# Kernel tuning notes

Measured on AMD Instinct MI355X. Metric: run time of the kernel, lower is better.

## Reference

```python
import jax, jax.numpy as jnp
import numpy as np

N_NODES = 50000
N_EDGES = 800000
HIDDEN = 128
N_LAYERS = 3
EPS = 1e-5


def setup_inputs() -> dict:
    key = jax.random.key(0)
    ks = jax.random.split(key, 6)
    x = jax.random.normal(ks[0], (N_NODES, HIDDEN), dtype=jnp.float32)
    edge_index = jax.random.randint(ks[1], (2, N_EDGES), 0, N_NODES, dtype=jnp.int64)
    scale = 1.0 / np.sqrt(HIDDEN)
    Wl = jax.random.normal(ks[2], (N_LAYERS, HIDDEN, HIDDEN), dtype=jnp.float32) * scale
    bl = jnp.zeros((N_LAYERS, HIDDEN), dtype=jnp.float32)
    Wr = jax.random.normal(ks[3], (N_LAYERS, HIDDEN, HIDDEN), dtype=jnp.float32) * scale
    gamma = jnp.ones((N_LAYERS, HIDDEN), dtype=jnp.float32)
    beta = jnp.zeros((N_LAYERS, HIDDEN), dtype=jnp.float32)
    return {"x": x, "edge_index": edge_index, "Wl": Wl, "bl": bl,
            "Wr": Wr, "gamma": gamma, "beta": beta}


def reference(x, edge_index, Wl, bl, Wr, gamma, beta):
    # SAGEConv (mean aggr): out_i = Wl @ mean_{j in N(i)} x_j + bl + Wr @ x_i
    # followed by BatchNorm (batch stats), ReLU, residual (layers > 0).
    src, dst = edge_index[0], edge_index[1]
    N = x.shape[0]
    deg = jax.ops.segment_sum(jnp.ones((src.shape[0],), dtype=x.dtype), dst,
                              num_segments=N)
    inv_deg = (1.0 / jnp.maximum(deg, 1.0))[:, None]  # [N,1]; empty nbhd -> 0 agg
    for i in range(N_LAYERS):
        msg = x[src]                                            # [E,H] gather
        agg = jax.ops.segment_sum(msg, dst, num_segments=N) * inv_deg  # [N,H]
        h = agg @ Wl[i].T + bl[i] + x @ Wr[i].T                 # [N,H]
        mean = jnp.mean(h, axis=0)
        var = jnp.var(h, axis=0)                                # biased, as torch BN
        h = gamma[i] * (h - mean) * jax.lax.rsqrt(var + EPS) + beta[i]
        h = jax.nn.relu(h)
        x = h + x if i > 0 else h
    return x
```

## Files before the change

kernel.cpp:

```cpp
#include <hip/hip_runtime.h>

#define HH 128
#define EPS 1e-5f
#define NBMAX 256
#define SCAP 40
#define FCAP 12288

typedef __bf16 bf16x8 __attribute__((ext_vector_type(8)));
typedef float f32x4 __attribute__((ext_vector_type(4)));
typedef float f32x2 __attribute__((ext_vector_type(2)));

__device__ __forceinline__ unsigned f2bf(float f) {
    unsigned u = __builtin_bit_cast(unsigned, f);
    return (u + 0x7FFFu + ((u >> 16) & 1u)) >> 16;
}
__device__ __forceinline__ float bflo(unsigned w) { return __builtin_bit_cast(float, w << 16); }
__device__ __forceinline__ float bfhi(unsigned w) { return __builtin_bit_cast(float, w & 0xFFFF0000u); }

__device__ __forceinline__ unsigned pack_fp8x4(float f0, float f1, float f2, float f3) {
    unsigned r = 0;
    r = __builtin_amdgcn_cvt_pk_fp8_f32(f0, f1, r, false);
    r = __builtin_amdgcn_cvt_pk_fp8_f32(f2, f3, r, true);
    return r;
}

__device__ __forceinline__ void gload_lds16(const void* g, void* l) {
    __builtin_amdgcn_global_load_lds(
        (const __attribute__((address_space(1))) unsigned int*)g,
        (__attribute__((address_space(3))) unsigned int*)l,
        16, 0, 0);
}

__global__ void zero_small_kernel(int* __restrict__ bcnt, float* __restrict__ stats3,
                                  unsigned* __restrict__ bar3) {
    const int t = threadIdx.x;
    bcnt[t] = 0;
    stats3[t] = 0.f; stats3[256 + t] = 0.f; stats3[512 + t] = 0.f;
    if (t < 3) bar3[t] = 0u;
}

__global__ __launch_bounds__(256) void bucket_hist_kernel(const int* __restrict__ dst,
                                                          int* __restrict__ bcnt, int E) {
    __shared__ int h[NBMAX];
    const int t = threadIdx.x;
    h[t] = 0;
    __syncthreads();
    for (int e = blockIdx.x * 256 + t; e < E; e += gridDim.x * 256)
        atomicAdd(&h[dst[e] >> 8], 1);
    __syncthreads();
    if (h[t]) atomicAdd(&bcnt[t], h[t]);
}

__global__ __launch_bounds__(256) void bucket_scan_kernel(const int* __restrict__ bcnt,
                                                          int* __restrict__ boff,
                                                          int* __restrict__ gpos, int NB, int E) {
    __shared__ int s[NBMAX];
    const int t = threadIdx.x;
    s[t] = (t < NB) ? bcnt[t] : 0;
    __syncthreads();
    for (int off = 1; off < 256; off <<= 1) {
        int u = (t >= off) ? s[t - off] : 0;
        __syncthreads();
        s[t] += u;
        __syncthreads();
    }
    int excl = (t == 0) ? 0 : s[t - 1];
    if (t < NB) { boff[t] = excl; gpos[t] = excl; }
    if (t == 0) boff[NB] = E;
}

__global__ __launch_bounds__(256) void bucket_scatter_kernel(
    const int* __restrict__ src, const int* __restrict__ dst,
    int* __restrict__ gpos, unsigned* __restrict__ packed, int E, int GRID)
{
    __shared__ unsigned q[NBMAX][SCAP];
    __shared__ int qc[NBMAX];
    const int t = threadIdx.x;
    const int b = blockIdx.x;
    qc[t] = 0;
    __syncthreads();
    const int ebeg = (int)((long)b * E / GRID);
    const int eend = (int)((long)(b + 1) * E / GRID);
    for (int base = ebeg; base < eend; base += 256) {
        int e = base + t;
        if (e < eend) {
            int d = dst[e];
            unsigned pk = ((unsigned)d << 16) | (unsigned)src[e];
            int bk = d >> 8;
            int slot = atomicAdd(&qc[bk], 1);
            if (slot < SCAP) q[bk][slot] = pk;
            else { int p = atomicAdd(&gpos[bk], 1); packed[p] = pk; }
        }
        __syncthreads();
        int c = qc[t]; if (c > SCAP) c = SCAP;
        if (c >= 32) {
            int p = atomicAdd(&gpos[t], 32);
            for (int i = 0; i < 32; ++i) packed[p + i] = q[t][i];
            for (int i = 32; i < c; ++i) q[t][i - 32] = q[t][i];
            qc[t] = c - 32;
        } else {
            qc[t] = c;
        }
        __syncthreads();
    }
    int c = qc[t]; if (c > SCAP) c = SCAP;
    if (c > 0) {
        int p = atomicAdd(&gpos[t], c);
        for (int i = 0; i < c; ++i) packed[p + i] = q[t][i];
    }
}

__global__ __launch_bounds__(256) void bucket_finalize_kernel(
    const unsigned* __restrict__ packed, const int* __restrict__ boff,
    int* __restrict__ row_ptr, float* __restrict__ invdeg,
    ushort* __restrict__ edge_csr, int N, int E)
{
    __shared__ int hist[256];
    __shared__ int posq[256];
    __shared__ ushort outq[FCAP];
    const int b = blockIdx.x, t = threadIdx.x;
    const int beg = boff[b], end = boff[b + 1], n = end - beg;
    hist[t] = 0;
    __syncthreads();
    for (int i = beg + t; i < end; i += 256)
        atomicAdd(&hist[(packed[i] >> 16) & 255], 1);
    __syncthreads();
    const int c = hist[t];
    for (int off = 1; off < 256; off <<= 1) {
        int u = (t >= off) ? hist[t - off] : 0;
        __syncthreads();
        hist[t] += u;
        __syncthreads();
    }
    const int excl = hist[t] - c;
    const int node = (b << 8) + t;
    if (node < N) {
        row_ptr[node] = beg + excl;
        invdeg[node] = 1.0f / fmaxf((float)c, 1.0f);
    }
    if (b == 0 && t == 0) row_ptr[N] = E;
    posq[t] = excl;
    __syncthreads();
    if (n <= FCAP) {
        for (int i = beg + t; i < end; i += 256) {
            unsigned pk = packed[i];
            int p = atomicAdd(&posq[(pk >> 16) & 255], 1);
            outq[p] = (ushort)(pk & 0xFFFFu);
        }
        __syncthreads();
        for (int i = t; i < n; i += 256) edge_csr[beg + i] = outq[i];
    } else {
        for (int i = beg + t; i < end; i += 256) {
            unsigned pk = packed[i];
            int p = atomicAdd(&posq[(pk >> 16) & 255], 1);
            edge_csr[beg + p] = (ushort)(pk & 0xFFFFu);
        }
    }
}

__global__ void convert_all_kernel(const float* __restrict__ x,
                                   const float* __restrict__ Wl, const float* __restrict__ Wr,
                                   ushort* __restrict__ xb, unsigned* __restrict__ xq,
                                   ushort* __restrict__ Wb,
                                   int n4, int m4, int wtotal) {
    int gid = blockIdx.x * 256 + threadIdx.x;
    if (gid < wtotal) {
        int l = gid / (HH * 256);
        int rem = gid - l * (HH * 256);
        int col = rem >> 8;
        int k = rem & 255;
        float v = (k < HH) ? Wl[(size_t)l * HH * HH + col * HH + k]
                           : Wr[(size_t)l * HH * HH + col * HH + (k - HH)];
        Wb[gid] = (ushort)f2bf(v);
        return;
    }
    int idx = gid - wtotal;
    if (idx >= m4) return;
    uint2 o = make_uint2(0u, 0u);
    unsigned q = 0u;
    if (idx < n4) {
        float4 v = ((const float4*)x)[idx];
        o.x = f2bf(v.x) | (f2bf(v.y) << 16);
        o.y = f2bf(v.z) | (f2bf(v.w) << 16);
        q = pack_fp8x4(v.x, v.y, v.z, v.w);
    }
    ((uint2*)xb)[idx] = o;
    xq[idx] = q;
}

__global__ __launch_bounds__(256) void gather_kernel(
    const unsigned* __restrict__ xq, const int* __restrict__ row_ptr,
    const ushort* __restrict__ edge_csr, const float* __restrict__ invdeg,
    ushort* __restrict__ aggb, int N)
{
    const int node = blockIdx.x * 16 + (threadIdx.x >> 4);
    const int l16 = threadIdx.x & 15;
    float a0=0,a1=0,a2=0,a3=0,a4=0,a5=0,a6=0,a7=0;
    float id = 0.f;
    if (node < N) {
        const int beg = row_ptr[node], end = row_ptr[node + 1];
        id = invdeg[node];
        int e = beg;
        for (; e + 3 < end; e += 4) {
            int s0 = edge_csr[e], s1 = edge_csr[e + 1];
            int s2 = edge_csr[e + 2], s3 = edge_csr[e + 3];
            uint2 v0 = *(const uint2*)(xq + (size_t)s0 * 32 + l16 * 2);
            uint2 v1 = *(const uint2*)(xq + (size_t)s1 * 32 + l16 * 2);
            uint2 v2 = *(const uint2*)(xq + (size_t)s2 * 32 + l16 * 2);
            uint2 v3 = *(const uint2*)(xq + (size_t)s3 * 32 + l16 * 2);
            f32x2 p;
            p = __builtin_amdgcn_cvt_pk_f32_fp8(v0.x, false); a0 += p.x; a1 += p.y;
            p = __builtin_amdgcn_cvt_pk_f32_fp8(v0.x, true);  a2 += p.x; a3 += p.y;
            p = __builtin_amdgcn_cvt_pk_f32_fp8(v0.y, false); a4 += p.x; a5 += p.y;
            p = __builtin_amdgcn_cvt_pk_f32_fp8(v0.y, true);  a6 += p.x; a7 += p.y;
            p = __builtin_amdgcn_cvt_pk_f32_fp8(v1.x, false); a0 += p.x; a1 += p.y;
            p = __builtin_amdgcn_cvt_pk_f32_fp8(v1.x, true);  a2 += p.x; a3 += p.y;
            p = __builtin_amdgcn_cvt_pk_f32_fp8(v1.y, false); a4 += p.x; a5 += p.y;
            p = __builtin_amdgcn_cvt_pk_f32_fp8(v1.y, true);  a6 += p.x; a7 += p.y;
            p = __builtin_amdgcn_cvt_pk_f32_fp8(v2.x, false); a0 += p.x; a1 += p.y;
            p = __builtin_amdgcn_cvt_pk_f32_fp8(v2.x, true);  a2 += p.x; a3 += p.y;
            p = __builtin_amdgcn_cvt_pk_f32_fp8(v2.y, false); a4 += p.x; a5 += p.y;
            p = __builtin_amdgcn_cvt_pk_f32_fp8(v2.y, true);  a6 += p.x; a7 += p.y;
            p = __builtin_amdgcn_cvt_pk_f32_fp8(v3.x, false); a0 += p.x; a1 += p.y;
            p = __builtin_amdgcn_cvt_pk_f32_fp8(v3.x, true);  a2 += p.x; a3 += p.y;
            p = __builtin_amdgcn_cvt_pk_f32_fp8(v3.y, false); a4 += p.x; a5 += p.y;
            p = __builtin_amdgcn_cvt_pk_f32_fp8(v3.y, true);  a6 += p.x; a7 += p.y;
        }
        for (; e < end; ++e) {
            int s0 = edge_csr[e];
            uint2 v0 = *(const uint2*)(xq + (size_t)s0 * 32 + l16 * 2);
            f32x2 p;
            p = __builtin_amdgcn_cvt_pk_f32_fp8(v0.x, false); a0 += p.x; a1 += p.y;
            p = __builtin_amdgcn_cvt_pk_f32_fp8(v0.x, true);  a2 += p.x; a3 += p.y;
            p = __builtin_amdgcn_cvt_pk_f32_fp8(v0.y, false); a4 += p.x; a5 += p.y;
            p = __builtin_amdgcn_cvt_pk_f32_fp8(v0.y, true);  a6 += p.x; a7 += p.y;
        }
    }
    uint4 o;
    o.x = f2bf(a0 * id) | (f2bf(a1 * id) << 16);
    o.y = f2bf(a2 * id) | (f2bf(a3 * id) << 16);
    o.z = f2bf(a4 * id) | (f2bf(a5 * id) << 16);
    o.w = f2bf(a6 * id) | (f2bf(a7 * id) << 16);
    *(uint4*)(aggb + (size_t)node * HH + l16 * 8) = o;
}

__global__ __launch_bounds__(512) void fused_layer_kernel(
    const ushort* __restrict__ aggb, ushort* __restrict__ xb,
    const ushort* __restrict__ Wb, const float* __restrict__ bl,
    const float* __restrict__ gamma, const float* __restrict__ beta,
    float* __restrict__ stats, unsigned* __restrict__ bar,
    unsigned* __restrict__ xq, float* __restrict__ outf,
    float invN, int nblocks, int N, int residual, int final_layer)
{
    extern __shared__ ushort As[];
    __shared__ float s_sum[128];
    __shared__ float s_sum2[128];

    const int tid = threadIdx.x;
    const int lane = tid & 63;
    const int wave = tid >> 6;
    const int m0 = blockIdx.x * 256;
    const int l15 = lane & 15;
    const int lg = lane >> 4;
    const int col = wave * 16 + l15;

#pragma unroll
    for (int i = 0; i < 16; ++i) {
        const int cb = (i * 8 + wave) * 64;
        const int L = cb + lane;
        const int r = L >> 5;
        const int c = L & 31;
        const int cs = (c & 0x18) | ((c & 7) ^ (r & 7));
        const ushort* gsrc = (cs < 16)
            ? (aggb + (size_t)(m0 + r) * HH + cs * 8)
            : (xb   + (size_t)(m0 + r) * HH + (cs - 16) * 8);
        gload_lds16(gsrc, &As[(size_t)cb * 8]);
    }

    bf16x8 bfr[8];
#pragma unroll
    for (int s = 0; s < 8; ++s)
        bfr[s] = *(const bf16x8*)(Wb + (size_t)col * 256 + s * 32 + lg * 8);

    if (tid < 128) { s_sum[tid] = 0.f; s_sum2[tid] = 0.f; }

    f32x4 acc[16];
#pragma unroll
    for (int rt = 0; rt < 16; ++rt) acc[rt] = (f32x4){0.f, 0.f, 0.f, 0.f};

    __syncthreads();

#pragma unroll
    for (int s = 0; s < 8; ++s) {
#pragma unroll
        for (int rt = 0; rt < 16; ++rt) {
            const int r = rt * 16 + l15;
            const int g = s * 4 + lg;
            const int c = (g & 0x18) | ((g & 7) ^ (r & 7));
            bf16x8 a = *(const bf16x8*)&As[r * 256 + c * 8];
            acc[rt] = __builtin_amdgcn_mfma_f32_16x16x32_bf16(a, bfr[s], acc[rt], 0, 0, 0);
        }
    }

    const float bias = bl[col];
    float s1 = 0.f, s2 = 0.f;
#pragma unroll
    for (int rt = 0; rt < 16; ++rt) {
#pragma unroll
        for (int r = 0; r < 4; ++r) {
            const int row = rt * 16 + lg * 4 + r;
            if (m0 + row < N) {
                float v = acc[rt][r] + bias;
                s1 += v; s2 += v * v;
            }
        }
    }
    atomicAdd(&s_sum[col], s1);
    atomicAdd(&s_sum2[col], s2);
    __syncthreads();
    if (tid < 128) {
        atomicAdd(&stats[tid], s_sum[tid]);
        atomicAdd(&stats[128 + tid], s_sum2[tid]);
    }
    if (tid == 0) {
        __threadfence();
        __hip_atomic_fetch_add(bar, 1u, __ATOMIC_ACQ_REL, __HIP_MEMORY_SCOPE_AGENT);
        while (__hip_atomic_load(bar, __ATOMIC_ACQUIRE, __HIP_MEMORY_SCOPE_AGENT) < (unsigned)nblocks)
            __builtin_amdgcn_s_sleep(8);
    }
    __syncthreads();

    const float sA = __hip_atomic_load(&stats[col], __ATOMIC_RELAXED, __HIP_MEMORY_SCOPE_AGENT);
    const float sB = __hip_atomic_load(&stats[128 + col], __ATOMIC_RELAXED, __HIP_MEMORY_SCOPE_AGENT);
    const float mean = sA * invN;
    const float var = sB * invN - mean * mean;
    const float aa = gamma[col] * rsqrtf(var + EPS);
    const float bb = beta[col] - mean * aa;

    ushort* Cs = As;
#pragma unroll
    for (int rt = 0; rt < 16; ++rt) {
#pragma unroll
        for (int r = 0; r < 4; ++r) {
            const int row = rt * 16 + lg * 4 + r;
            float v = acc[rt][r] + bias;
            float o = fmaxf(fmaf(v, aa, bb), 0.f);
            Cs[row * 136 + col] = (ushort)f2bf(o);
        }
    }
    __syncthreads();

#pragma unroll
    for (int i = 0; i < 8; ++i) {
        const int ch = tid + i * 512;
        const int row = ch >> 4;
        const int q = ch & 15;
        const int grow = m0 + row;
        if (grow < N) {
            uint4 v = *(const uint4*)&Cs[row * 136 + q * 8];
            float o0 = bflo(v.x), o1 = bfhi(v.x);
            float o2 = bflo(v.y), o3 = bfhi(v.y);
            float o4 = bflo(v.z), o5 = bfhi(v.z);
            float o6 = bflo(v.w), o7 = bfhi(v.w);
            if (residual) {
                uint4 xw = *(const uint4*)(xb + (size_t)grow * HH + q * 8);
                o0 += bflo(xw.x); o1 += bfhi(xw.x);
                o2 += bflo(xw.y); o3 += bfhi(xw.y);
                o4 += bflo(xw.z); o5 += bfhi(xw.z);
                o6 += bflo(xw.w); o7 += bfhi(xw.w);
            }
            if (final_layer) {
                float* op = outf + (size_t)grow * HH + q * 8;
                *(float4*)op = make_float4(o0, o1, o2, o3);
                *(float4*)(op + 4) = make_float4(o4, o5, o6, o7);
            } else {
                uint4 ob;
                ob.x = f2bf(o0) | (f2bf(o1) << 16);
                ob.y = f2bf(o2) | (f2bf(o3) << 16);
                ob.z = f2bf(o4) | (f2bf(o5) << 16);
                ob.w = f2bf(o6) | (f2bf(o7) << 16);
                *(uint4*)(xb + (size_t)grow * HH + q * 8) = ob;
                uint2 qb;
                qb.x = pack_fp8x4(o0, o1, o2, o3);
                qb.y = pack_fp8x4(o4, o5, o6, o7);
                *(uint2*)(xq + (size_t)grow * 32 + q * 2) = qb;
            }
        }
    }
}

extern "C" void kernel_launch(void* const* d_in, const int* in_sizes, int n_in,
                              void* d_out, int out_size, void* d_ws, size_t ws_size,
                              hipStream_t stream) {
    const float* x     = (const float*)d_in[0];
    const int*   ei    = (const int*)d_in[1];
    const float* Wl    = (const float*)d_in[2];
    const float* bl    = (const float*)d_in[3];
    const float* Wr    = (const float*)d_in[4];
    const float* gamma = (const float*)d_in[5];
    const float* beta  = (const float*)d_in[6];
    float* out = (float*)d_out;

    const int N = in_sizes[0] / HH;
    const int E = in_sizes[1] / 2;
    const int MP = ((N + 255) / 256) * 256;
    const int NB = (N + 255) >> 8;
    const int* src = ei;
    const int* dst = ei + E;

    char* p = (char*)d_ws;
    ushort* aggb    = (ushort*)p; p += (size_t)MP * HH * 2;
    ushort* xb      = (ushort*)p; p += (size_t)MP * HH * 2;
    unsigned* xq    = (unsigned*)p; p += (size_t)MP * 32 * 4;
    ushort* Wb      = (ushort*)p; p += (size_t)3 * HH * 256 * 2;
    float* invdeg   = (float*)p;  p += (size_t)N * 4;
    float* stats3   = (float*)p;  p += 768 * 4;
    unsigned* bar3  = (unsigned*)p; p += 16 * 4;
    int* row_ptr    = (int*)p;    p += (size_t)(N + 4) * 4;
    int* bcnt       = (int*)p;    p += NBMAX * 4;
    int* boff       = (int*)p;    p += (NBMAX + 1) * 4;
    int* gpos       = (int*)p;    p += NBMAX * 4;
    unsigned* packed = (unsigned*)p; p += (size_t)E * 4;
    ushort* edge_csr = (ushort*)p;  p += (size_t)((E + 7) & ~7) * 2;

    hipFuncSetAttribute((const void*)fused_layer_kernel,
                        hipFuncAttributeMaxDynamicSharedMemorySize, 131072);

    zero_small_kernel<<<1, 256, 0, stream>>>(bcnt, stats3, bar3);
    bucket_hist_kernel<<<512, 256, 0, stream>>>(dst, bcnt, E);
    bucket_scan_kernel<<<1, 256, 0, stream>>>(bcnt, boff, gpos, NB, E);
    bucket_scatter_kernel<<<256, 256, 0, stream>>>(src, dst, gpos, packed, E, 256);
    bucket_finalize_kernel<<<NB, 256, 0, stream>>>(packed, boff, row_ptr, invdeg, edge_csr, N, E);

    const int wtotal = 3 * HH * 256;
    const int n4 = N * (HH / 4);
    const int m4 = MP * (HH / 4);
    convert_all_kernel<<<(wtotal + m4 + 255) / 256, 256, 0, stream>>>(
        x, Wl, Wr, xb, xq, Wb, n4, m4, wtotal);

    const int gather_blocks = MP / 16;
    const int fused_blocks = MP / 256;

    for (int layer = 0; layer < 3; ++layer) {
        gather_kernel<<<gather_blocks, 256, 0, stream>>>(
            xq, row_ptr, edge_csr, invdeg, aggb, N);

        fused_layer_kernel<<<fused_blocks, 512, 131072, stream>>>(
            aggb, xb, Wb + (size_t)layer * HH * 256, bl + (size_t)layer * HH,
            gamma + (size_t)layer * HH, beta + (size_t)layer * HH,
            stats3 + layer * 256, bar3 + layer,
            xq, out, 1.0f / (float)N, fused_blocks, N,
            layer > 0 ? 1 : 0, layer == 2 ? 1 : 0);
    }
}
```

Before: 223.3 us.

## Merge CSR build and conversion prologue into one persistent kernel with grid barriers

```diff
diff --git a/kernel.cpp b/kernel.cpp
--- a/kernel.cpp
+++ b/kernel.cpp
@@ -5,6 +5,7 @@
 #define NBMAX 256
 #define SCAP 40
 #define FCAP 12288
+#define MGRID 256
 
 typedef __bf16 bf16x8 __attribute__((ext_vector_type(8)));
 typedef float f32x4 __attribute__((ext_vector_type(4)));
@@ -31,161 +32,176 @@
         16, 0, 0);
 }
 
+__device__ __forceinline__ void grid_barrier(unsigned* ctr, unsigned nb) {
+    __syncthreads();
+    if (threadIdx.x == 0) {
+        __threadfence();
+        __hip_atomic_fetch_add(ctr, 1u, __ATOMIC_ACQ_REL, __HIP_MEMORY_SCOPE_AGENT);
+        while (__hip_atomic_load(ctr, __ATOMIC_ACQUIRE, __HIP_MEMORY_SCOPE_AGENT) < nb)
+            __builtin_amdgcn_s_sleep(8);
+    }
+    __syncthreads();
+}
+
+__device__ __forceinline__ int aload(const int* p) {
+    return __hip_atomic_load((int*)p, __ATOMIC_RELAXED, __HIP_MEMORY_SCOPE_AGENT);
+}
+
 __global__ void zero_small_kernel(int* __restrict__ bcnt, float* __restrict__ stats3,
-                                  unsigned* __restrict__ bar3) {
+                                  unsigned* __restrict__ bar) {
     const int t = threadIdx.x;
     bcnt[t] = 0;
     stats3[t] = 0.f; stats3[256 + t] = 0.f; stats3[512 + t] = 0.f;
-    if (t < 3) bar3[t] = 0u;
-}
-
-__global__ __launch_bounds__(256) void bucket_hist_kernel(const int* __restrict__ dst,
-                                                          int* __restrict__ bcnt, int E) {
-    __shared__ int h[NBMAX];
-    const int t = threadIdx.x;
-    h[t] = 0;
-    __syncthreads();
-    for (int e = blockIdx.x * 256 + t; e < E; e += gridDim.x * 256)
-        atomicAdd(&h[dst[e] >> 8], 1);
-    __syncthreads();
-    if (h[t]) atomicAdd(&bcnt[t], h[t]);
-}
-
-__global__ __launch_bounds__(256) void bucket_scan_kernel(const int* __restrict__ bcnt,
-                                                          int* __restrict__ boff,
-                                                          int* __restrict__ gpos, int NB, int E) {
-    __shared__ int s[NBMAX];
-    const int t = threadIdx.x;
-    s[t] = (t < NB) ? bcnt[t] : 0;
-    __syncthreads();
-    for (int off = 1; off < 256; off <<= 1) {
-        int u = (t >= off) ? s[t - off] : 0;
-        __syncthreads();
-        s[t] += u;
-        __syncthreads();
-    }
-    int excl = (t == 0) ? 0 : s[t - 1];
-    if (t < NB) { boff[t] = excl; gpos[t] = excl; }
-    if (t == 0) boff[NB] = E;
-}
-
-__global__ __launch_bounds__(256) void bucket_scatter_kernel(
+    if (t < 8) bar[t] = 0u;
+}
+
+__global__ __launch_bounds__(256) void mega_prologue_kernel(
+    const float* __restrict__ x, const float* __restrict__ Wl, const float* __restrict__ Wr,
     const int* __restrict__ src, const int* __restrict__ dst,
-    int* __restrict__ gpos, unsigned* __restrict__ packed, int E, int GRID)
+    ushort* __restrict__ xb, unsigned* __restrict__ xq, ushort* __restrict__ Wb,
+    int* __restrict__ bcnt, int* __restrict__ boff, int* __restrict__ gpos,
+    unsigned* __restrict__ packed, int* __restrict__ row_ptr,
+    float* __restrict__ invdeg, ushort* __restrict__ edge_csr,
+    unsigned* __restrict__ bar,
+    int n4, int m4, int wtotal, int N, int E, int NB)
 {
-    __shared__ unsigned q[NBMAX][SCAP];
-    __shared__ int qc[NBMAX];
+    __shared__ char smraw[NBMAX * SCAP * 4 + NBMAX * 4];
     const int t = threadIdx.x;
     const int b = blockIdx.x;
-    qc[t] = 0;
-    __syncthreads();
-    const int ebeg = (int)((long)b * E / GRID);
-    const int eend = (int)((long)(b + 1) * E / GRID);
-    for (int base = ebeg; base < eend; base += 256) {
-        int e = base + t;
-        if (e < eend) {
-            int d = dst[e];
-            unsigned pk = ((unsigned)d << 16) | (unsigned)src[e];
-            int bk = d >> 8;
-            int slot = atomicAdd(&qc[bk], 1);
-            if (slot < SCAP) q[bk][slot] = pk;
-            else { int p = atomicAdd(&gpos[bk], 1); packed[p] = pk; }
-        }
-        __syncthreads();
-        int c = qc[t]; if (c > SCAP) c = SCAP;
-        if (c >= 32) {
-            int p = atomicAdd(&gpos[t], 32);
-            for (int i = 0; i < 32; ++i) packed[p + i] = q[t][i];
-            for (int i = 32; i < c; ++i) q[t][i - 32] = q[t][i];
-            qc[t] = c - 32;
-        } else {
-            qc[t] = c;
-        }
-        __syncthreads();
-    }
-    int c = qc[t]; if (c > SCAP) c = SCAP;
-    if (c > 0) {
-        int p = atomicAdd(&gpos[t], c);
-        for (int i = 0; i < c; ++i) packed[p + i] = q[t][i];
-    }
-}
-
-__global__ __launch_bounds__(256) void bucket_finalize_kernel(
-    const unsigned* __restrict__ packed, const int* __restrict__ boff,
-    int* __restrict__ row_ptr, float* __restrict__ invdeg,
-    ushort* __restrict__ edge_csr, int N, int E)
-{
-    __shared__ int hist[256];
-    __shared__ int posq[256];
-    __shared__ ushort outq[FCAP];
-    const int b = blockIdx.x, t = threadIdx.x;
-    const int beg = boff[b], end = boff[b + 1], n = end - beg;
-    hist[t] = 0;
-    __syncthreads();
-    for (int i = beg + t; i < end; i += 256)
-        atomicAdd(&hist[(packed[i] >> 16) & 255], 1);
-    __syncthreads();
-    const int c = hist[t];
-    for (int off = 1; off < 256; off <<= 1) {
-        int u = (t >= off) ? hist[t - off] : 0;
-        __syncthreads();
-        hist[t] += u;
-        __syncthreads();
-    }
-    const int excl = hist[t] - c;
-    const int node = (b << 8) + t;
-    if (node < N) {
-        row_ptr[node] = beg + excl;
-        invdeg[node] = 1.0f / fmaxf((float)c, 1.0f);
-    }
-    if (b == 0 && t == 0) row_ptr[N] = E;
-    posq[t] = excl;
-    __syncthreads();
-    if (n <= FCAP) {
-        for (int i = beg + t; i < end; i += 256) {
-            unsigned pk = packed[i];
-            int p = atomicAdd(&posq[(pk >> 16) & 255], 1);
-            outq[p] = (ushort)(pk & 0xFFFFu);
-        }
-        __syncthreads();
-        for (int i = t; i < n; i += 256) edge_csr[beg + i] = outq[i];
-    } else {
-        for (int i = beg + t; i < end; i += 256) {
-            unsigned pk = packed[i];
-            int p = atomicAdd(&posq[(pk >> 16) & 255], 1);
-            edge_csr[beg + p] = (ushort)(pk & 0xFFFFu);
-        }
-    }
-}
-
-__global__ void convert_all_kernel(const float* __restrict__ x,
-                                   const float* __restrict__ Wl, const float* __restrict__ Wr,
-                                   ushort* __restrict__ xb, unsigned* __restrict__ xq,
-                                   ushort* __restrict__ Wb,
-                                   int n4, int m4, int wtotal) {
-    int gid = blockIdx.x * 256 + threadIdx.x;
-    if (gid < wtotal) {
-        int l = gid / (HH * 256);
-        int rem = gid - l * (HH * 256);
+    const int gt = b * 256 + t;
+    const int gstride = MGRID * 256;
+
+    {
+        int* h0 = (int*)smraw;
+        h0[t] = 0;
+        __syncthreads();
+        for (int e = gt; e < E; e += gstride) atomicAdd(&h0[dst[e] >> 8], 1);
+        __syncthreads();
+        if (h0[t]) atomicAdd(&bcnt[t], h0[t]);
+    }
+    for (int i = gt; i < wtotal; i += gstride) {
+        int l = i / (HH * 256);
+        int rem = i - l * (HH * 256);
         int col = rem >> 8;
         int k = rem & 255;
         float v = (k < HH) ? Wl[(size_t)l * HH * HH + col * HH + k]
                            : Wr[(size_t)l * HH * HH + col * HH + (k - HH)];
-        Wb[gid] = (ushort)f2bf(v);
-        return;
-    }
-    int idx = gid - wtotal;
-    if (idx >= m4) return;
-    uint2 o = make_uint2(0u, 0u);
-    unsigned q = 0u;
-    if (idx < n4) {
-        float4 v = ((const float4*)x)[idx];
-        o.x = f2bf(v.x) | (f2bf(v.y) << 16);
-        o.y = f2bf(v.z) | (f2bf(v.w) << 16);
-        q = pack_fp8x4(v.x, v.y, v.z, v.w);
-    }
-    ((uint2*)xb)[idx] = o;
-    xq[idx] = q;
+        Wb[i] = (ushort)f2bf(v);
+    }
+    for (int i = gt; i < m4; i += gstride) {
+        uint2 o = make_uint2(0u, 0u);
+        unsigned qv = 0u;
+        if (i < n4) {
+            float4 v = ((const float4*)x)[i];
+            o.x = f2bf(v.x) | (f2bf(v.y) << 16);
+            o.y = f2bf(v.z) | (f2bf(v.w) << 16);
+            qv = pack_fp8x4(v.x, v.y, v.z, v.w);
+        }
+        ((uint2*)xb)[i] = o;
+        xq[i] = qv;
+    }
+
+    grid_barrier(bar + 0, MGRID);
+
+    if (b == 0) {
+        int* s = (int*)smraw;
+        s[t] = (t < NB) ? aload(&bcnt[t]) : 0;
+        __syncthreads();
+        for (int off = 1; off < 256; off <<= 1) {
+            int u = (t >= off) ? s[t - off] : 0;
+            __syncthreads();
+            s[t] += u;
+            __syncthreads();
+        }
+        int excl = (t == 0) ? 0 : s[t - 1];
+        if (t < NB) { boff[t] = excl; gpos[t] = excl; }
+        if (t == 0) boff[NB] = E;
+    }
+
+    grid_barrier(bar + 1, MGRID);
+
+    {
+        unsigned (*q)[SCAP] = (unsigned (*)[SCAP])smraw;
+        int* qc = (int*)(smraw + NBMAX * SCAP * 4);
+        qc[t] = 0;
+        __syncthreads();
+        const int ebeg = (int)((long)b * E / MGRID);
+        const int eend = (int)((long)(b + 1) * E / MGRID);
+        for (int base = ebeg; base < eend; base += 256) {
+            int e = base + t;
+            if (e < eend) {
+                int d = dst[e];
+                unsigned pk = ((unsigned)d << 16) | (unsigned)src[e];
+                int bk = d >> 8;
+                int slot = atomicAdd(&qc[bk], 1);
+                if (slot < SCAP) q[bk][slot] = pk;
+                else { int p = atomicAdd(&gpos[bk], 1); packed[p] = pk; }
+            }
+            __syncthreads();
+            int c = qc[t]; if (c > SCAP) c = SCAP;
+            if (c >= 32) {
+                int p = atomicAdd(&gpos[t], 32);
+                for (int i = 0; i < 32; ++i) packed[p + i] = q[t][i];
+                for (int i = 32; i < c; ++i) q[t][i - 32] = q[t][i];
+                qc[t] = c - 32;
+            } else {
+                qc[t] = c;
+            }
+            __syncthreads();
+        }
+        int c = qc[t]; if (c > SCAP) c = SCAP;
+        if (c > 0) {
+            int p = atomicAdd(&gpos[t], c);
+            for (int i = 0; i < c; ++i) packed[p + i] = q[t][i];
+        }
+    }
+
+    grid_barrier(bar + 2, MGRID);
+
+    if (b < NB) {
+        int* hist = (int*)smraw;
+        int* posq = hist + 256;
+        ushort* outq = (ushort*)(posq + 256);
+        const int beg = aload(&boff[b]);
+        const int end = aload(&boff[b + 1]);
+        const int n = end - beg;
+        hist[t] = 0;
+        __syncthreads();
+        for (int i = beg + t; i < end; i += 256)
+            atomicAdd(&hist[(packed[i] >> 16) & 255], 1);
+        __syncthreads();
+        const int c = hist[t];
+        for (int off = 1; off < 256; off <<= 1) {
+            int u = (t >= off) ? hist[t - off] : 0;
+            __syncthreads();
+            hist[t] += u;
+            __syncthreads();
+        }
+        const int excl = hist[t] - c;
+        const int node = (b << 8) + t;
+        if (node < N) {
+            row_ptr[node] = beg + excl;
+            invdeg[node] = 1.0f / fmaxf((float)c, 1.0f);
+        }
+        if (b == 0 && t == 0) row_ptr[N] = E;
+        posq[t] = excl;
+        __syncthreads();
+        if (n <= FCAP) {
+            for (int i = beg + t; i < end; i += 256) {
+                unsigned pk = packed[i];
+                int p = atomicAdd(&posq[(pk >> 16) & 255], 1);
+                outq[p] = (ushort)(pk & 0xFFFFu);
+            }
+            __syncthreads();
+            for (int i = t; i < n; i += 256) edge_csr[beg + i] = outq[i];
+        } else {
+            for (int i = beg + t; i < end; i += 256) {
+                unsigned pk = packed[i];
+                int p = atomicAdd(&posq[(pk >> 16) & 255], 1);
+                edge_csr[beg + p] = (ushort)(pk & 0xFFFFu);
+            }
+        }
+    }
 }
 
 __global__ __launch_bounds__(256) void gather_kernel(
@@ -415,7 +431,7 @@
     ushort* Wb      = (ushort*)p; p += (size_t)3 * HH * 256 * 2;
     float* invdeg   = (float*)p;  p += (size_t)N * 4;
     float* stats3   = (float*)p;  p += 768 * 4;
-    unsigned* bar3  = (unsigned*)p; p += 16 * 4;
+    unsigned* bar   = (unsigned*)p; p += 16 * 4;
     int* row_ptr    = (int*)p;    p += (size_t)(N + 4) * 4;
     int* bcnt       = (int*)p;    p += NBMAX * 4;
     int* boff       = (int*)p;    p += (NBMAX + 1) * 4;
@@ -426,17 +442,15 @@
     hipFuncSetAttribute((const void*)fused_layer_kernel,
                         hipFuncAttributeMaxDynamicSharedMemorySize, 131072);
 
-    zero_small_kernel<<<1, 256, 0, stream>>>(bcnt, stats3, bar3);
-    bucket_hist_kernel<<<512, 256, 0, stream>>>(dst, bcnt, E);
-    bucket_scan_kernel<<<1, 256, 0, stream>>>(bcnt, boff, gpos, NB, E);
-    bucket_scatter_kernel<<<256, 256, 0, stream>>>(src, dst, gpos, packed, E, 256);
-    bucket_finalize_kernel<<<NB, 256, 0, stream>>>(packed, boff, row_ptr, invdeg, edge_csr, N, E);
-
     const int wtotal = 3 * HH * 256;
     const int n4 = N * (HH / 4);
     const int m4 = MP * (HH / 4);
-    convert_all_kernel<<<(wtotal + m4 + 255) / 256, 256, 0, stream>>>(
-        x, Wl, Wr, xb, xq, Wb, n4, m4, wtotal);
+
+    zero_small_kernel<<<1, 256, 0, stream>>>(bcnt, stats3, bar);
+    mega_prologue_kernel<<<MGRID, 256, 0, stream>>>(
+        x, Wl, Wr, src, dst, xb, xq, Wb,
+        bcnt, boff, gpos, packed, row_ptr, invdeg, edge_csr,
+        bar, n4, m4, wtotal, N, E, NB);
 
     const int gather_blocks = MP / 16;
     const int fused_blocks = MP / 256;
@@ -448,7 +462,7 @@
         fused_layer_kernel<<<fused_blocks, 512, 131072, stream>>>(
             aggb, xb, Wb + (size_t)layer * HH * 256, bl + (size_t)layer * HH,
             gamma + (size_t)layer * HH, beta + (size_t)layer * HH,
-            stats3 + layer * 256, bar3 + layer,
+            stats3 + layer * 256, bar + 3 + layer,
             xq, out, 1.0f / (float)N, fused_blocks, N,
             layer > 0 ? 1 : 0, layer == 2 ? 1 : 0);
     }
```

Measured after the change: 295.5 us. 1.32x slower.
